# Kernel tuning notes

Measured on AMD Instinct MI355X. Metric: run time of the kernel, lower is better.

Reference implementation:

```python
import jax, jax.numpy as jnp
import numpy as np

N, E, B = 30000, 60000, 500          # nodes, edges, graphs
NODE_IN, EDGE_IN, H, R = 64, 16, 64, 1024
MP_STEPS, S2S_STEPS = 3, 3           # num_step_message_passing, num_step_set2set
D = 2 * H                            # Set2Set in_channels / LSTM hidden size


def setup_inputs() -> dict:
    key = jax.random.key(0)
    ks = jax.random.split(key, 20)
    g = lambda i, shape, s: jax.random.normal(ks[i], shape, jnp.float32) * s
    return {
        "x": g(0, (N, NODE_IN), 1.0),
        "edge_index": jax.random.randint(ks[1], (2, E), 0, N),
        "edge_attr": g(2, (E, EDGE_IN), 1.0),
        "batch": jnp.sort(jax.random.randint(ks[3], (N,), 0, B)),
        # project_node_feats
        "W_proj": g(4, (NODE_IN, H), 0.1), "b_proj": jnp.zeros((H,), jnp.float32),
        # NNConv edge network + root + bias
        "W_edge": g(5, (EDGE_IN, H * H), 0.05), "b_edge": jnp.zeros((H * H,), jnp.float32),
        "root": g(6, (H, H), 0.1), "conv_bias": jnp.zeros((H,), jnp.float32),
        # GRU (torch gate order r, z, n)
        "gru_W_ih": g(7, (3 * H, H), 0.1), "gru_W_hh": g(8, (3 * H, H), 0.1),
        "gru_b_ih": jnp.zeros((3 * H,), jnp.float32), "gru_b_hh": jnp.zeros((3 * H,), jnp.float32),
        # node classifier head
        "W_cls": g(9, (H, 1), 0.1), "b_cls": jnp.zeros((1,), jnp.float32),
        # Set2Set LSTM: input 2D (=4H), hidden D (=2H), gate order i, f, g, o
        "lstm_W_ih": g(10, (4 * D, 2 * D), 0.1), "lstm_W_hh": g(11, (4 * D, D), 0.1),
        "lstm_b_ih": jnp.zeros((4 * D,), jnp.float32), "lstm_b_hh": jnp.zeros((4 * D,), jnp.float32),
        # sparsify (Linear 4H->R + PReLU)
        "W_sp": g(12, (4 * H, R), 0.05), "b_sp": jnp.zeros((R,), jnp.float32),
        "prelu_a": jnp.float32(0.25),
        "W_y1": g(13, (R, 128), 0.05), "b_y1": jnp.zeros((128,), jnp.float32),
        "W_y2": g(14, (128, 1), 0.1), "b_y2": jnp.zeros((1,), jnp.float32),
    }


def reference(x, edge_index, edge_attr, batch,
              W_proj, b_proj, W_edge, b_edge, root, conv_bias,
              gru_W_ih, gru_W_hh, gru_b_ih, gru_b_hh,
              W_cls, b_cls,
              lstm_W_ih, lstm_W_hh, lstm_b_ih, lstm_b_hh,
              W_sp, b_sp, prelu_a, W_y1, b_y1, W_y2, b_y2):
    src, dst = edge_index[0], edge_index[1]
    h0 = jax.nn.relu(x @ W_proj + b_proj)                  # [N, H]
    # Per-edge HxH weight matrices (loop-invariant; NNConv recomputes same values).
    We = (edge_attr @ W_edge + b_edge).reshape(E, H, H)    # [E, H, H]

    node, hidden = h0, h0
    for _ in range(MP_STEPS):
        msg = jnp.einsum('eh,eho->eo', node[src], We)      # gather + per-edge matvec
        aggr = jax.ops.segment_sum(msg, dst, num_segments=N)
        m = jax.nn.relu(aggr + node @ root + conv_bias)    # NNConv output + activation
        # GRU cell (seq_len=1)
        gi = m @ gru_W_ih.T + gru_b_ih
        gh = hidden @ gru_W_hh.T + gru_b_hh
        r = jax.nn.sigmoid(gi[:, :H] + gh[:, :H])
        z = jax.nn.sigmoid(gi[:, H:2 * H] + gh[:, H:2 * H])
        n = jnp.tanh(gi[:, 2 * H:] + r * gh[:, 2 * H:])
        hidden = (1.0 - z) * n + z * hidden
        node = hidden

    xcat = jnp.concatenate([h0, node], axis=1)             # [N, 2H] = [N, D]
    p_borylation = (node @ W_cls + b_cls)[:, 0]            # [N]

    # Set2Set over xcat
    q_star = jnp.zeros((B, 2 * D), xcat.dtype)
    hs = jnp.zeros((B, D), xcat.dtype)
    cs = jnp.zeros((B, D), xcat.dtype)
    for _ in range(S2S_STEPS):
        gts = q_star @ lstm_W_ih.T + lstm_b_ih + hs @ lstm_W_hh.T + lstm_b_hh
        i_g = jax.nn.sigmoid(gts[:, :D])
        f_g = jax.nn.sigmoid(gts[:, D:2 * D])
        g_g = jnp.tanh(gts[:, 2 * D:3 * D])
        o_g = jax.nn.sigmoid(gts[:, 3 * D:])
        cs = f_g * cs + i_g * g_g
        hs = o_g * jnp.tanh(cs)
        q = hs                                             # [B, D]
        e = jnp.sum(xcat * q[batch], axis=-1)              # [N]
        mseg = jax.ops.segment_max(e, batch, num_segments=B)
        ex = jnp.exp(e - mseg[batch])
        denom = jax.ops.segment_sum(ex, batch, num_segments=B)
        a = ex / denom[batch]                              # segment softmax
        rvec = jax.ops.segment_sum(a[:, None] * xcat, batch, num_segments=B)
        q_star = jnp.concatenate([q, rvec], axis=1)        # [B, 2D] = [B, 4H]

    gf = q_star @ W_sp + b_sp
    gf = jnp.where(gf >= 0, gf, prelu_a * gf)              # PReLU
    predicted_yield = (jax.nn.relu(gf @ W_y1 + b_y1) @ W_y2 + b_y2)[:, 0]
    return p_borylation, predicted_yield
```

## Files before the change

kernel.cpp:

```cpp
#include <hip/hip_runtime.h>
#include <math.h>

#define NN 30000
#define NNP 30080
#define NE 60000
#define NB 500
#define YROW 1344

typedef __attribute__((ext_vector_type(8))) short bf16x8;
typedef __attribute__((ext_vector_type(4))) float f32x4;

__device__ __forceinline__ float sigmoidf_(float x) { return 1.0f / (1.0f + expf(-x)); }

__device__ __forceinline__ unsigned short bf_hi(float x) {
  unsigned int u = __float_as_uint(x);
  u += 0x7FFF + ((u >> 16) & 1);
  return (unsigned short)(u >> 16);
}
__device__ __forceinline__ float bf_f(unsigned short h) {
  return __uint_as_float(((unsigned int)h) << 16);
}
__device__ __forceinline__ void split_bf(float x, unsigned short& hi, unsigned short& lo) {
  hi = bf_hi(x);
  lo = bf_hi(x - bf_f(hi));
}

__device__ __forceinline__ int lower_bound_i(const int* __restrict__ a, int n, int v) {
  int lo = 0, hi = n;
  while (lo < hi) { int mid = (lo + hi) >> 1; if (a[mid] < v) lo = mid + 1; else hi = mid; }
  return lo;
}

__global__ __launch_bounds__(256) void gemm_mfma_k(
    const unsigned short* __restrict__ Ahi, const unsigned short* __restrict__ Alo,
    const unsigned short* __restrict__ Bhi, const unsigned short* __restrict__ Blo,
    float* __restrict__ C, int ldc,
    float* __restrict__ C2,
    unsigned short* __restrict__ Chi, unsigned short* __restrict__ Clo,
    const float* __restrict__ bias, int M, int flags)
{
  const int tid = threadIdx.x;
  const int wid = tid >> 6, lane = tid & 63;
  const int l15 = lane & 15, l4 = lane >> 4;
  const int r0 = blockIdx.x * 128 + (wid >> 1) * 64;
  const int c0 = blockIdx.y * 64 + (wid & 1) * 32;

  f32x4 acc[4][2];
#pragma unroll
  for (int rt = 0; rt < 4; rt++)
#pragma unroll
    for (int ct = 0; ct < 2; ct++) acc[rt][ct] = (f32x4){0.f, 0.f, 0.f, 0.f};

#pragma unroll
  for (int ks = 0; ks < 2; ks++) {
    const int kb = ks * 32 + l4 * 8;
    bf16x8 a_h[4], a_l[4], b_h[2], b_l[2];
#pragma unroll
    for (int rt = 0; rt < 4; rt++) {
      size_t off = (size_t)(r0 + rt * 16 + l15) * 64 + kb;
      a_h[rt] = *(const bf16x8*)(Ahi + off);
      a_l[rt] = *(const bf16x8*)(Alo + off);
    }
#pragma unroll
    for (int ct = 0; ct < 2; ct++) {
      size_t off = (size_t)(c0 + ct * 16 + l15) * 64 + kb;
      b_h[ct] = *(const bf16x8*)(Bhi + off);
      b_l[ct] = *(const bf16x8*)(Blo + off);
    }
#pragma unroll
    for (int rt = 0; rt < 4; rt++)
#pragma unroll
      for (int ct = 0; ct < 2; ct++) {
        acc[rt][ct] = __builtin_amdgcn_mfma_f32_16x16x32_bf16(a_h[rt], b_h[ct], acc[rt][ct], 0, 0, 0);
        acc[rt][ct] = __builtin_amdgcn_mfma_f32_16x16x32_bf16(a_h[rt], b_l[ct], acc[rt][ct], 0, 0, 0);
        acc[rt][ct] = __builtin_amdgcn_mfma_f32_16x16x32_bf16(a_l[rt], b_h[ct], acc[rt][ct], 0, 0, 0);
      }
  }

#pragma unroll
  for (int rt = 0; rt < 4; rt++) {
    const int rbase = r0 + rt * 16 + l4 * 4;
#pragma unroll
    for (int ct = 0; ct < 2; ct++) {
      const int col = c0 + ct * 16 + l15;
      const float bv = (flags & 1) ? bias[col] : 0.f;
#pragma unroll
      for (int reg = 0; reg < 4; reg++) {
        const int row = rbase + reg;
        if (row < M) {
          float v = acc[rt][ct][reg];
          if (flags & 1) v = fmaxf(v + bv, 0.f);
          C[(size_t)row * ldc + col] = v;
          if (flags & 4) C2[(size_t)row * 64 + col] = v;
          if (flags & 2) {
            unsigned short h, l;
            split_bf(v, h, l);
            Chi[(size_t)row * 64 + col] = h;
            Clo[(size_t)row * 64 + col] = l;
          }
        }
      }
    }
  }
}

__global__ __launch_bounds__(256) void prep_bt_k(
    const float* __restrict__ W_edge, const float* __restrict__ b_edge,
    const float* __restrict__ root, const float* __restrict__ gWhh,
    const float* __restrict__ gWih, const float* __restrict__ W_proj,
    unsigned short* __restrict__ BTbig_hi, unsigned short* __restrict__ BTbig_lo,
    unsigned short* __restrict__ BTih_hi, unsigned short* __restrict__ BTih_lo,
    unsigned short* __restrict__ BTp_hi, unsigned short* __restrict__ BTp_lo)
{
  int idx = blockIdx.x * 256 + threadIdx.x;
  const int NBIG = YROW * 64, NIH = 192 * 64, NP = 64 * 64;
  if (idx < NBIG) {
    int col = idx >> 6, k = idx & 63;
    float v;
    if (col < 1024) { int c = col >> 6, o2 = col & 63; v = W_edge[(size_t)c * 4096 + k * 64 + o2]; }
    else if (col < 1088) v = b_edge[k * 64 + (col - 1024)];
    else if (col < 1152) v = root[k * 64 + (col - 1088)];
    else v = gWhh[(size_t)(col - 1152) * 64 + k];
    unsigned short h, l; split_bf(v, h, l);
    BTbig_hi[idx] = h; BTbig_lo[idx] = l;
  } else if (idx < NBIG + NIH) {
    int i2 = idx - NBIG;
    float v = gWih[i2];
    unsigned short h, l; split_bf(v, h, l);
    BTih_hi[i2] = h; BTih_lo[i2] = l;
  } else if (idx < NBIG + NIH + NP) {
    int i2 = idx - NBIG - NIH;
    int o2 = i2 >> 6, k = i2 & 63;
    float v = W_proj[k * 64 + o2];
    unsigned short h, l; split_bf(v, h, l);
    BTp_hi[i2] = h; BTp_lo[i2] = l;
  }
}

__global__ __launch_bounds__(256) void prep_lstmT_k(
    const float* __restrict__ Wih, const float* __restrict__ Whh,
    float* __restrict__ Tih, float* __restrict__ Thh)
{
  int idx = blockIdx.x * 256 + threadIdx.x;
  if (idx < 256 * 512) {
    int j = idx / 512, r = idx % 512;
    Tih[idx] = Wih[(size_t)r * 256 + j];
  } else if (idx < 256 * 512 + 128 * 512) {
    int id2 = idx - 256 * 512;
    int j = id2 / 512, r = id2 % 512;
    Thh[id2] = Whh[(size_t)r * 128 + j];
  }
}

__global__ __launch_bounds__(256) void split2_k(
    const float* __restrict__ src, unsigned short* __restrict__ hi,
    unsigned short* __restrict__ lo, int n4)
{
  int i = blockIdx.x * 256 + threadIdx.x;
  if (i >= n4) return;
  float4 v = ((const float4*)src)[i];
  unsigned short h0, l0, h1, l1, h2, l2, h3, l3;
  split_bf(v.x, h0, l0); split_bf(v.y, h1, l1);
  split_bf(v.z, h2, l2); split_bf(v.w, h3, l3);
  ((ushort4*)hi)[i] = make_ushort4(h0, h1, h2, h3);
  ((ushort4*)lo)[i] = make_ushort4(l0, l1, l2, l3);
}

__global__ __launch_bounds__(256) void edge_msg_k(
    const int* __restrict__ ei, const float* __restrict__ ea, float* __restrict__ Yb)
{
  int gw = (blockIdx.x * blockDim.x + threadIdx.x) >> 6;
  if (gw >= NE) return;
  int lane = threadIdx.x & 63;
  int src = ei[gw];
  int dst = ei[NE + gw];
  const float* y = Yb + (size_t)src * YROW;
  const float* eav = ea + (size_t)gw * 16;
  float4 e0 = *(const float4*)(eav + 0);
  float4 e1 = *(const float4*)(eav + 4);
  float4 e2 = *(const float4*)(eav + 8);
  float4 e3 = *(const float4*)(eav + 12);
  float msg = y[1024 + lane];
  msg = fmaf(e0.x, y[0 * 64 + lane], msg);  msg = fmaf(e0.y, y[1 * 64 + lane], msg);
  msg = fmaf(e0.z, y[2 * 64 + lane], msg);  msg = fmaf(e0.w, y[3 * 64 + lane], msg);
  msg = fmaf(e1.x, y[4 * 64 + lane], msg);  msg = fmaf(e1.y, y[5 * 64 + lane], msg);
  msg = fmaf(e1.z, y[6 * 64 + lane], msg);  msg = fmaf(e1.w, y[7 * 64 + lane], msg);
  msg = fmaf(e2.x, y[8 * 64 + lane], msg);  msg = fmaf(e2.y, y[9 * 64 + lane], msg);
  msg = fmaf(e2.z, y[10 * 64 + lane], msg); msg = fmaf(e2.w, y[11 * 64 + lane], msg);
  msg = fmaf(e3.x, y[12 * 64 + lane], msg); msg = fmaf(e3.y, y[13 * 64 + lane], msg);
  msg = fmaf(e3.z, y[14 * 64 + lane], msg); msg = fmaf(e3.w, y[15 * 64 + lane], msg);
  atomicAdd(&Yb[(size_t)dst * YROW + 1088 + lane], msg);
}

__global__ __launch_bounds__(256) void m_relu_split_k(
    const float* __restrict__ Yb, const float* __restrict__ conv_b,
    unsigned short* __restrict__ mbh, unsigned short* __restrict__ mbl)
{
  int t = blockIdx.x * 256 + threadIdx.x;
  if (t >= NN * 64) return;
  int n = t >> 6, c = t & 63;
  float v = fmaxf(Yb[(size_t)n * YROW + 1088 + c] + conv_b[c], 0.f);
  unsigned short h, l; split_bf(v, h, l);
  mbh[t] = h; mbl[t] = l;
}

__global__ __launch_bounds__(256) void gru_split_k(
    const float* __restrict__ gi, const float* __restrict__ Yb,
    const float* __restrict__ bih, const float* __restrict__ bhh,
    float* __restrict__ h, unsigned short* __restrict__ hh, unsigned short* __restrict__ hl)
{
  int t = blockIdx.x * 256 + threadIdx.x;
  if (t >= NN * 64) return;
  int n = t >> 6, c = t & 63;
  const float* gin = gi + (size_t)n * 192;
  const float* ghn = Yb + (size_t)n * YROW + 1152;
  float r = sigmoidf_(gin[c] + bih[c] + ghn[c] + bhh[c]);
  float z = sigmoidf_(gin[64 + c] + bih[64 + c] + ghn[64 + c] + bhh[64 + c]);
  float ng = tanhf(gin[128 + c] + bih[128 + c] + r * (ghn[128 + c] + bhh[128 + c]));
  float hv = h[t];
  float hn = (1.f - z) * ng + z * hv;
  h[t] = hn;
  unsigned short hb, lb; split_bf(hn, hb, lb);
  hh[t] = hb; hl[t] = lb;
}

__global__ __launch_bounds__(256) void cls_xcat_k(
    const float* __restrict__ h, const float* __restrict__ Wcls,
    const float* __restrict__ bcls, float* __restrict__ xcat, float* __restrict__ out)
{
  int gw = (blockIdx.x * blockDim.x + threadIdx.x) >> 6;
  if (gw >= NN) return;
  int lane = threadIdx.x & 63;
  float hv = h[(size_t)gw * 64 + lane];
  xcat[(size_t)gw * 128 + 64 + lane] = hv;
  float p = hv * Wcls[lane];
#pragma unroll
  for (int off = 32; off > 0; off >>= 1) p += __shfl_xor(p, off);
  if (lane == 0) out[gw] = p + bcls[0];
}

__global__ __launch_bounds__(256) void gemmK_k(
    const float* __restrict__ A, int lda,
    const float* __restrict__ B, int ldb,
    float* __restrict__ C, int ldc,
    const float* __restrict__ Csrc,
    const float* __restrict__ bias, const float* __restrict__ alpha_p,
    int M, int K, int flags)
{
  __shared__ float As[64 * 68];
  __shared__ float Bs[64 * 64];
  const int tid = threadIdx.x;
  const int m0 = blockIdx.x * 64;
  const int n0 = blockIdx.y * 64;
  const int tx = tid & 15, ty = tid >> 4;
  float acc[4][4] = {};

  for (int kc = 0; kc < K; kc += 64) {
#pragma unroll
    for (int i = 0; i < 4; i++) {
      int f4 = tid + i * 256;
      int row = f4 >> 4;
      int kk = (f4 & 15) << 2;
      float4 v = make_float4(0.f, 0.f, 0.f, 0.f);
      if (m0 + row < M) v = *(const float4*)(A + (size_t)(m0 + row) * lda + kc + kk);
      *(float4*)&As[row * 68 + kk] = v;
    }
#pragma unroll
    for (int i = 0; i < 4; i++) {
      int f4 = tid + i * 256;
      int kk = f4 >> 4;
      int nn = (f4 & 15) << 2;
      float4 v = *(const float4*)(B + (size_t)(kc + kk) * ldb + n0 + nn);
      *(float4*)&Bs[kk * 64 + nn] = v;
    }
    __syncthreads();
    const float* As0 = As + (ty * 4 + 0) * 68;
    const float* As1 = As + (ty * 4 + 1) * 68;
    const float* As2 = As + (ty * 4 + 2) * 68;
    const float* As3 = As + (ty * 4 + 3) * 68;
#pragma unroll
    for (int k = 0; k < 64; k++) {
      float4 b = *(const float4*)(Bs + k * 64 + tx * 4);
      float a0 = As0[k], a1 = As1[k], a2 = As2[k], a3 = As3[k];
      acc[0][0] = fmaf(a0, b.x, acc[0][0]); acc[0][1] = fmaf(a0, b.y, acc[0][1]);
      acc[0][2] = fmaf(a0, b.z, acc[0][2]); acc[0][3] = fmaf(a0, b.w, acc[0][3]);
      acc[1][0] = fmaf(a1, b.x, acc[1][0]); acc[1][1] = fmaf(a1, b.y, acc[1][1]);
      acc[1][2] = fmaf(a1, b.z, acc[1][2]); acc[1][3] = fmaf(a1, b.w, acc[1][3]);
      acc[2][0] = fmaf(a2, b.x, acc[2][0]); acc[2][1] = fmaf(a2, b.y, acc[2][1]);
      acc[2][2] = fmaf(a2, b.z, acc[2][2]); acc[2][3] = fmaf(a2, b.w, acc[2][3]);
      acc[3][0] = fmaf(a3, b.x, acc[3][0]); acc[3][1] = fmaf(a3, b.y, acc[3][1]);
      acc[3][2] = fmaf(a3, b.z, acc[3][2]); acc[3][3] = fmaf(a3, b.w, acc[3][3]);
    }
    __syncthreads();
  }

  const int coln = tx * 4;
  const int col = n0 + coln;
  float alpha = (flags & 32) ? alpha_p[0] : 0.f;
#pragma unroll
  for (int i = 0; i < 4; i++) {
    int row = m0 + ty * 4 + i;
    if (row < M) {
      float v0 = acc[i][0], v1 = acc[i][1], v2 = acc[i][2], v3 = acc[i][3];
      size_t off = (size_t)row * ldc + col;
      if (flags & 4) {
        float4 s = *(const float4*)(Csrc + off);
        v0 += s.x; v1 += s.y; v2 += s.z; v3 += s.w;
      }
      if (flags & 1) {
        v0 += bias[col + 0]; v1 += bias[col + 1]; v2 += bias[col + 2]; v3 += bias[col + 3];
      }
      if (flags & 2) {
        v0 = fmaxf(v0, 0.f); v1 = fmaxf(v1, 0.f); v2 = fmaxf(v2, 0.f); v3 = fmaxf(v3, 0.f);
      }
      if (flags & 32) {
        v0 = (v0 >= 0.f) ? v0 : alpha * v0; v1 = (v1 >= 0.f) ? v1 : alpha * v1;
        v2 = (v2 >= 0.f) ? v2 : alpha * v2; v3 = (v3 >= 0.f) ? v3 : alpha * v3;
      }
      *(float4*)&C[off] = make_float4(v0, v1, v2, v3);
    }
  }
}

__global__ __launch_bounds__(256) void lstm_elem_k(
    const float* __restrict__ gts, const float* __restrict__ bih, const float* __restrict__ bhh,
    float* __restrict__ hs, float* __restrict__ cs)
{
  int t = blockIdx.x * 256 + threadIdx.x;
  if (t >= NB * 128) return;
  int b = t >> 7, d = t & 127;
  const float* g = gts + (size_t)b * 512;
  float iv = sigmoidf_(g[d] + bih[d] + bhh[d]);
  float fv = sigmoidf_(g[128 + d] + bih[128 + d] + bhh[128 + d]);
  float gv = tanhf(g[256 + d] + bih[256 + d] + bhh[256 + d]);
  float ov = sigmoidf_(g[384 + d] + bih[384 + d] + bhh[384 + d]);
  float c = fv * cs[t] + iv * gv;
  cs[t] = c;
  hs[t] = ov * tanhf(c);
}

__global__ __launch_bounds__(256) void attn_k(
    const float* __restrict__ xcat, const int* __restrict__ batch,
    const float* __restrict__ hs, float* __restrict__ e_ws, float* __restrict__ q_star)
{
  __shared__ float q[128];
  __shared__ float red[4];
  __shared__ float rvw[4 * 128];
  __shared__ float dw[4];
  __shared__ int se[2];
  int b = blockIdx.x;
  int tid = threadIdx.x;
  if (tid < 128) q[tid] = hs[(size_t)b * 128 + tid];
  if (tid == 254) se[0] = lower_bound_i(batch, NN, b);
  if (tid == 255) se[1] = lower_bound_i(batch, NN, b + 1);
  __syncthreads();
  int start = se[0], end = se[1];
  int lane = tid & 63, w = tid >> 6;
  float wmax = -INFINITY;
  for (int n = start + w; n < end; n += 4) {
    const float* xr = xcat + (size_t)n * 128;
    float p = xr[lane] * q[lane] + xr[64 + lane] * q[64 + lane];
#pragma unroll
    for (int off = 32; off > 0; off >>= 1) p += __shfl_xor(p, off);
    if (lane == 0) e_ws[n] = p;
    wmax = fmaxf(wmax, p);
  }
  if (lane == 0) red[w] = wmax;
  __syncthreads();
  float bmax = fmaxf(fmaxf(red[0], red[1]), fmaxf(red[2], red[3]));
  float a0 = 0.f, a1 = 0.f, ds = 0.f;
  for (int n = start + w; n < end; n += 4) {
    float ex = expf(e_ws[n] - bmax);
    const float* xr = xcat + (size_t)n * 128;
    a0 = fmaf(ex, xr[lane], a0);
    a1 = fmaf(ex, xr[64 + lane], a1);
    ds += ex;
  }
  rvw[w * 128 + lane] = a0;
  rvw[w * 128 + 64 + lane] = a1;
  if (lane == 0) dw[w] = ds;
  __syncthreads();
  if (tid < 128) {
    float r = rvw[tid] + rvw[128 + tid] + rvw[256 + tid] + rvw[384 + tid];
    float dsum = dw[0] + dw[1] + dw[2] + dw[3];
    q_star[(size_t)b * 256 + tid] = q[tid];
    q_star[(size_t)b * 256 + 128 + tid] = (end > start) ? (r / dsum) : 0.f;
  }
}

__global__ __launch_bounds__(256) void yout_k(
    const float* __restrict__ y1, const float* __restrict__ Wy2,
    const float* __restrict__ by2, float* __restrict__ out)
{
  int gw = (blockIdx.x * blockDim.x + threadIdx.x) >> 6;
  if (gw >= NB) return;
  int lane = threadIdx.x & 63;
  const float* yr = y1 + (size_t)gw * 128;
  float p = yr[lane] * Wy2[lane] + yr[64 + lane] * Wy2[64 + lane];
#pragma unroll
  for (int off = 32; off > 0; off >>= 1) p += __shfl_xor(p, off);
  if (lane == 0) out[gw] = p + by2[0];
}

extern "C" void kernel_launch(void* const* d_in, const int* in_sizes, int n_in,
                              void* d_out, int out_size, void* d_ws, size_t ws_size,
                              hipStream_t stream) {
  const float* x      = (const float*)d_in[0];
  const int*   ei     = (const int*)d_in[1];
  const float* ea     = (const float*)d_in[2];
  const int*   batch  = (const int*)d_in[3];
  const float* W_proj = (const float*)d_in[4];
  const float* b_proj = (const float*)d_in[5];
  const float* W_edge = (const float*)d_in[6];
  const float* b_edge = (const float*)d_in[7];
  const float* root   = (const float*)d_in[8];
  const float* conv_b = (const float*)d_in[9];
  const float* gWih   = (const float*)d_in[10];
  const float* gWhh   = (const float*)d_in[11];
  const float* gbih   = (const float*)d_in[12];
  const float* gbhh   = (const float*)d_in[13];
  const float* Wcls   = (const float*)d_in[14];
  const float* bcls   = (const float*)d_in[15];
  const float* lWih   = (const float*)d_in[16];
  const float* lWhh   = (const float*)d_in[17];
  const float* lbih   = (const float*)d_in[18];
  const float* lbhh   = (const float*)d_in[19];
  const float* Wsp    = (const float*)d_in[20];
  const float* bsp    = (const float*)d_in[21];
  const float* pa     = (const float*)d_in[22];
  const float* Wy1    = (const float*)d_in[23];
  const float* by1    = (const float*)d_in[24];
  const float* Wy2    = (const float*)d_in[25];
  const float* by2    = (const float*)d_in[26];
  float* out = (float*)d_out;

  float* ws = (float*)d_ws;
  size_t o = 0;
  float* h      = ws + o; o += (size_t)NN * 64;
  float* Ybig   = ws + o; o += (size_t)NN * YROW;
  float* gi     = ws + o; o += (size_t)NN * 192;
  float* xcat   = ws + o; o += (size_t)NN * 128;
  float* e_ws   = ws + o; o += (size_t)NN;
  float* q_star = ws + o; o += (size_t)NB * 256;
  float* hs     = ws + o; o += (size_t)NB * 128;
  float* cs     = ws + o; o += (size_t)NB * 128;
  float* Tih    = ws + o; o += 256 * 512;
  float* Thh    = ws + o; o += 128 * 512;
  float* gts    = ws + o; o += (size_t)NB * 512;
  float* gf     = ws + o; o += (size_t)NB * 1024;
  float* y1     = ws + o; o += (size_t)NB * 128;

  unsigned short* us = (unsigned short*)(ws + o);
  size_t u = 0;
  unsigned short* hh_b   = us + u; u += (size_t)NNP * 64;
  unsigned short* hl_b   = us + u; u += (size_t)NNP * 64;
  unsigned short* mbh    = us + u; u += (size_t)NNP * 64;
  unsigned short* mbl    = us + u; u += (size_t)NNP * 64;
  unsigned short* BTb_hi = us + u; u += (size_t)YROW * 64;
  unsigned short* BTb_lo = us + u; u += (size_t)YROW * 64;
  unsigned short* BTi_hi = us + u; u += (size_t)192 * 64;
  unsigned short* BTi_lo = us + u; u += (size_t)192 * 64;
  unsigned short* BTp_hi = us + u; u += (size_t)64 * 64;
  unsigned short* BTp_lo = us + u; u += (size_t)64 * 64;

  const int MT = NNP / 128;

  prep_bt_k<<<((YROW + 192 + 64) * 64 + 255) / 256, 256, 0, stream>>>(
      W_edge, b_edge, root, gWhh, gWih, W_proj,
      BTb_hi, BTb_lo, BTi_hi, BTi_lo, BTp_hi, BTp_lo);
  prep_lstmT_k<<<768, 256, 0, stream>>>(lWih, lWhh, Tih, Thh);
  split2_k<<<(NN * 16 + 255) / 256, 256, 0, stream>>>(x, hh_b, hl_b, NN * 16);

  gemm_mfma_k<<<dim3(MT, 1), 256, 0, stream>>>(hh_b, hl_b, BTp_hi, BTp_lo,
                                               xcat, 128, h, hh_b, hl_b, b_proj, NN, 1 | 2 | 4);
  for (int step = 0; step < 3; step++) {
    gemm_mfma_k<<<dim3(MT, YROW / 64), 256, 0, stream>>>(hh_b, hl_b, BTb_hi, BTb_lo,
                                                         Ybig, YROW, nullptr, nullptr, nullptr,
                                                         nullptr, NN, 0);
    edge_msg_k<<<(NE * 64) / 256, 256, 0, stream>>>(ei, ea, Ybig);
    m_relu_split_k<<<(NN * 64) / 256, 256, 0, stream>>>(Ybig, conv_b, mbh, mbl);
    gemm_mfma_k<<<dim3(MT, 3), 256, 0, stream>>>(mbh, mbl, BTi_hi, BTi_lo,
                                                 gi, 192, nullptr, nullptr, nullptr,
                                                 nullptr, NN, 0);
    gru_split_k<<<(NN * 64) / 256, 256, 0, stream>>>(gi, Ybig, gbih, gbhh, h, hh_b, hl_b);
  }
  cls_xcat_k<<<(NN * 64) / 256, 256, 0, stream>>>(h, Wcls, bcls, xcat, out);
  hipMemsetAsync(q_star, 0, (size_t)NB * (256 + 128 + 128) * sizeof(float), stream);
  for (int t = 0; t < 3; t++) {
    gemmK_k<<<dim3(8, 8), 256, 0, stream>>>(q_star, 256, Tih, 512, gts, 512,
                                            nullptr, nullptr, nullptr, NB, 256, 0);
    gemmK_k<<<dim3(8, 8), 256, 0, stream>>>(hs, 128, Thh, 512, gts, 512,
                                            gts, nullptr, nullptr, NB, 128, 4);
    lstm_elem_k<<<(NB * 128 + 255) / 256, 256, 0, stream>>>(gts, lbih, lbhh, hs, cs);
    attn_k<<<NB, 256, 0, stream>>>(xcat, batch, hs, e_ws, q_star);
  }
  gemmK_k<<<dim3(8, 16), 256, 0, stream>>>(q_star, 256, Wsp, 1024, gf, 1024,
                                           nullptr, bsp, pa, NB, 256, 1 | 32);
  gemmK_k<<<dim3(8, 2), 256, 0, stream>>>(gf, 1024, Wy1, 128, y1, 128,
                                          nullptr, by1, nullptr, NB, 1024, 1 | 2);
  yout_k<<<(NB * 64 + 255) / 256, 256, 0, stream>>>(y1, Wy2, by2, out + NN);
}
```

Baseline: 807.8 us.

## Compute NNConv messages per edge with MFMA instead of a per-node 1344-wide GEMM

Before, every node was multiplied by a 64x1344 weight matrix to produce per-channel projections, and each edge then gathered a 1344-float row. Now the node GEMM is cut to root plus GRU hidden (256 columns). A new edge kernel builds an outer-product operand (edge_attr times source h, K=1088) and multiplies it by the reordered edge-network weights with split-bf16 MFMA, then scatters the result with atomics. This removes the large Ybig write and read traffic. In exchange it adds about twice the MFMA FLOPs over edges and per-edge gathers of h.

```diff
diff --git a/kernel.cpp b/kernel.cpp
--- a/kernel.cpp
+++ b/kernel.cpp
@@ -5,7 +5,8 @@
 #define NNP 30080
 #define NE 60000
 #define NB 500
-#define YROW 1344
+#define YGH 256
+#define KE 1088
 
 typedef __attribute__((ext_vector_type(8))) short bf16x8;
 typedef __attribute__((ext_vector_type(4))) float f32x4;
@@ -104,32 +105,113 @@
   }
 }
 
+__global__ __launch_bounds__(256) void edge_mfma_k(
+    const int* __restrict__ ei, const float* __restrict__ ea,
+    const float* __restrict__ h,
+    const unsigned short* __restrict__ Whi, const unsigned short* __restrict__ Wlo,
+    float* __restrict__ Yb)
+{
+  const int tid = threadIdx.x;
+  const int wid = tid >> 6, lane = tid & 63;
+  const int l15 = lane & 15, l4 = lane >> 4;
+  const int e0 = (blockIdx.x * 4 + wid) * 64;
+
+  int srcA[4];
+  const float* eaA[4];
+#pragma unroll
+  for (int rt = 0; rt < 4; rt++) {
+    int e = e0 + rt * 16 + l15;
+    int ee = (e < NE) ? e : (NE - 1);
+    srcA[rt] = ei[ee];
+    eaA[rt] = ea + (size_t)ee * 16;
+  }
+
+  f32x4 acc[4][4];
+#pragma unroll
+  for (int rt = 0; rt < 4; rt++)
+#pragma unroll
+    for (int ct = 0; ct < 4; ct++) acc[rt][ct] = (f32x4){0.f, 0.f, 0.f, 0.f};
+
+  for (int ks = 0; ks < KE / 32; ks++) {
+    const int base = ks * 32 + l4 * 8;
+    const int c = base >> 6;
+    const int kb = base & 63;
+    bf16x8 ah[4], al[4];
+#pragma unroll
+    for (int rt = 0; rt < 4; rt++) {
+      float eac = (c < 16) ? eaA[rt][c] : 1.0f;
+      const float* hp = h + (size_t)srcA[rt] * 64 + kb;
+      float4 n0 = *(const float4*)hp;
+      float4 n1 = *(const float4*)(hp + 4);
+      float nv[8] = {n0.x, n0.y, n0.z, n0.w, n1.x, n1.y, n1.z, n1.w};
+#pragma unroll
+      for (int j = 0; j < 8; j++) {
+        unsigned short hb, lb;
+        split_bf(eac * nv[j], hb, lb);
+        ah[rt][j] = (short)hb;
+        al[rt][j] = (short)lb;
+      }
+    }
+#pragma unroll
+    for (int ct = 0; ct < 4; ct++) {
+      size_t wo = (size_t)(ct * 16 + l15) * KE + base;
+      bf16x8 bh = *(const bf16x8*)(Whi + wo);
+      bf16x8 bl = *(const bf16x8*)(Wlo + wo);
+#pragma unroll
+      for (int rt = 0; rt < 4; rt++) {
+        acc[rt][ct] = __builtin_amdgcn_mfma_f32_16x16x32_bf16(ah[rt], bh, acc[rt][ct], 0, 0, 0);
+        acc[rt][ct] = __builtin_amdgcn_mfma_f32_16x16x32_bf16(ah[rt], bl, acc[rt][ct], 0, 0, 0);
+        acc[rt][ct] = __builtin_amdgcn_mfma_f32_16x16x32_bf16(al[rt], bh, acc[rt][ct], 0, 0, 0);
+      }
+    }
+  }
+
+#pragma unroll
+  for (int rt = 0; rt < 4; rt++) {
+    const int er = e0 + rt * 16 + l4 * 4;
+#pragma unroll
+    for (int reg = 0; reg < 4; reg++) {
+      const int e = er + reg;
+      if (e < NE) {
+        const int dst = ei[NE + e];
+#pragma unroll
+        for (int ct = 0; ct < 4; ct++)
+          atomicAdd(&Yb[(size_t)dst * YGH + ct * 16 + l15], acc[rt][ct][reg]);
+      }
+    }
+  }
+}
+
 __global__ __launch_bounds__(256) void prep_bt_k(
     const float* __restrict__ W_edge, const float* __restrict__ b_edge,
     const float* __restrict__ root, const float* __restrict__ gWhh,
     const float* __restrict__ gWih, const float* __restrict__ W_proj,
     unsigned short* __restrict__ BTbig_hi, unsigned short* __restrict__ BTbig_lo,
+    unsigned short* __restrict__ W2_hi, unsigned short* __restrict__ W2_lo,
     unsigned short* __restrict__ BTih_hi, unsigned short* __restrict__ BTih_lo,
     unsigned short* __restrict__ BTp_hi, unsigned short* __restrict__ BTp_lo)
 {
   int idx = blockIdx.x * 256 + threadIdx.x;
-  const int NBIG = YROW * 64, NIH = 192 * 64, NP = 64 * 64;
+  const int NBIG = YGH * 64, NW2 = 64 * KE, NIH = 192 * 64, NP = 64 * 64;
   if (idx < NBIG) {
     int col = idx >> 6, k = idx & 63;
-    float v;
-    if (col < 1024) { int c = col >> 6, o2 = col & 63; v = W_edge[(size_t)c * 4096 + k * 64 + o2]; }
-    else if (col < 1088) v = b_edge[k * 64 + (col - 1024)];
-    else if (col < 1152) v = root[k * 64 + (col - 1088)];
-    else v = gWhh[(size_t)(col - 1152) * 64 + k];
+    float v = (col < 64) ? root[k * 64 + col] : gWhh[(size_t)(col - 64) * 64 + k];
     unsigned short h, l; split_bf(v, h, l);
     BTbig_hi[idx] = h; BTbig_lo[idx] = l;
-  } else if (idx < NBIG + NIH) {
+  } else if (idx < NBIG + NW2) {
     int i2 = idx - NBIG;
+    int o2 = i2 / KE, kq = i2 % KE;
+    int c = kq >> 6, kk = kq & 63;
+    float v = (c < 16) ? W_edge[(size_t)c * 4096 + kk * 64 + o2] : b_edge[kk * 64 + o2];
+    unsigned short h, l; split_bf(v, h, l);
+    W2_hi[i2] = h; W2_lo[i2] = l;
+  } else if (idx < NBIG + NW2 + NIH) {
+    int i2 = idx - NBIG - NW2;
     float v = gWih[i2];
     unsigned short h, l; split_bf(v, h, l);
     BTih_hi[i2] = h; BTih_lo[i2] = l;
-  } else if (idx < NBIG + NIH + NP) {
-    int i2 = idx - NBIG - NIH;
+  } else if (idx < NBIG + NW2 + NIH + NP) {
+    int i2 = idx - NBIG - NW2 - NIH;
     int o2 = i2 >> 6, k = i2 & 63;
     float v = W_proj[k * 64 + o2];
     unsigned short h, l; split_bf(v, h, l);
@@ -166,32 +248,6 @@
   ((ushort4*)lo)[i] = make_ushort4(l0, l1, l2, l3);
 }
 
-__global__ __launch_bounds__(256) void edge_msg_k(
-    const int* __restrict__ ei, const float* __restrict__ ea, float* __restrict__ Yb)
-{
-  int gw = (blockIdx.x * blockDim.x + threadIdx.x) >> 6;
-  if (gw >= NE) return;
-  int lane = threadIdx.x & 63;
-  int src = ei[gw];
-  int dst = ei[NE + gw];
-  const float* y = Yb + (size_t)src * YROW;
-  const float* eav = ea + (size_t)gw * 16;
-  float4 e0 = *(const float4*)(eav + 0);
-  float4 e1 = *(const float4*)(eav + 4);
-  float4 e2 = *(const float4*)(eav + 8);
-  float4 e3 = *(const float4*)(eav + 12);
-  float msg = y[1024 + lane];
-  msg = fmaf(e0.x, y[0 * 64 + lane], msg);  msg = fmaf(e0.y, y[1 * 64 + lane], msg);
-  msg = fmaf(e0.z, y[2 * 64 + lane], msg);  msg = fmaf(e0.w, y[3 * 64 + lane], msg);
-  msg = fmaf(e1.x, y[4 * 64 + lane], msg);  msg = fmaf(e1.y, y[5 * 64 + lane], msg);
-  msg = fmaf(e1.z, y[6 * 64 + lane], msg);  msg = fmaf(e1.w, y[7 * 64 + lane], msg);
-  msg = fmaf(e2.x, y[8 * 64 + lane], msg);  msg = fmaf(e2.y, y[9 * 64 + lane], msg);
-  msg = fmaf(e2.z, y[10 * 64 + lane], msg); msg = fmaf(e2.w, y[11 * 64 + lane], msg);
-  msg = fmaf(e3.x, y[12 * 64 + lane], msg); msg = fmaf(e3.y, y[13 * 64 + lane], msg);
-  msg = fmaf(e3.z, y[14 * 64 + lane], msg); msg = fmaf(e3.w, y[15 * 64 + lane], msg);
-  atomicAdd(&Yb[(size_t)dst * YROW + 1088 + lane], msg);
-}
-
 __global__ __launch_bounds__(256) void m_relu_split_k(
     const float* __restrict__ Yb, const float* __restrict__ conv_b,
     unsigned short* __restrict__ mbh, unsigned short* __restrict__ mbl)
@@ -199,7 +255,7 @@
   int t = blockIdx.x * 256 + threadIdx.x;
   if (t >= NN * 64) return;
   int n = t >> 6, c = t & 63;
-  float v = fmaxf(Yb[(size_t)n * YROW + 1088 + c] + conv_b[c], 0.f);
+  float v = fmaxf(Yb[(size_t)n * YGH + c] + conv_b[c], 0.f);
   unsigned short h, l; split_bf(v, h, l);
   mbh[t] = h; mbl[t] = l;
 }
@@ -213,7 +269,7 @@
   if (t >= NN * 64) return;
   int n = t >> 6, c = t & 63;
   const float* gin = gi + (size_t)n * 192;
-  const float* ghn = Yb + (size_t)n * YROW + 1152;
+  const float* ghn = Yb + (size_t)n * YGH + 64;
   float r = sigmoidf_(gin[c] + bih[c] + ghn[c] + bhh[c]);
   float z = sigmoidf_(gin[64 + c] + bih[64 + c] + ghn[64 + c] + bhh[64 + c]);
   float ng = tanhf(gin[128 + c] + bih[128 + c] + r * (ghn[128 + c] + bhh[128 + c]));
@@ -437,7 +493,7 @@
   float* ws = (float*)d_ws;
   size_t o = 0;
   float* h      = ws + o; o += (size_t)NN * 64;
-  float* Ybig   = ws + o; o += (size_t)NN * YROW;
+  float* Ybig   = ws + o; o += (size_t)NN * YGH;
   float* gi     = ws + o; o += (size_t)NN * 192;
   float* xcat   = ws + o; o += (size_t)NN * 128;
   float* e_ws   = ws + o; o += (size_t)NN;
@@ -456,28 +512,32 @@
   unsigned short* hl_b   = us + u; u += (size_t)NNP * 64;
   unsigned short* mbh    = us + u; u += (size_t)NNP * 64;
   unsigned short* mbl    = us + u; u += (size_t)NNP * 64;
-  unsigned short* BTb_hi = us + u; u += (size_t)YROW * 64;
-  unsigned short* BTb_lo = us + u; u += (size_t)YROW * 64;
+  unsigned short* BTb_hi = us + u; u += (size_t)YGH * 64;
+  unsigned short* BTb_lo = us + u; u += (size_t)YGH * 64;
+  unsigned short* W2_hi  = us + u; u += (size_t)64 * KE;
+  unsigned short* W2_lo  = us + u; u += (size_t)64 * KE;
   unsigned short* BTi_hi = us + u; u += (size_t)192 * 64;
   unsigned short* BTi_lo = us + u; u += (size_t)192 * 64;
   unsigned short* BTp_hi = us + u; u += (size_t)64 * 64;
   unsigned short* BTp_lo = us + u; u += (size_t)64 * 64;
 
   const int MT = NNP / 128;
-
-  prep_bt_k<<<((YROW + 192 + 64) * 64 + 255) / 256, 256, 0, stream>>>(
+  const int ET = (NE + 255) / 256;
+  const int PREP_N = YGH * 64 + 64 * KE + 192 * 64 + 64 * 64;
+
+  prep_bt_k<<<(PREP_N + 255) / 256, 256, 0, stream>>>(
       W_edge, b_edge, root, gWhh, gWih, W_proj,
-      BTb_hi, BTb_lo, BTi_hi, BTi_lo, BTp_hi, BTp_lo);
+      BTb_hi, BTb_lo, W2_hi, W2_lo, BTi_hi, BTi_lo, BTp_hi, BTp_lo);
   prep_lstmT_k<<<768, 256, 0, stream>>>(lWih, lWhh, Tih, Thh);
   split2_k<<<(NN * 16 + 255) / 256, 256, 0, stream>>>(x, hh_b, hl_b, NN * 16);
 
   gemm_mfma_k<<<dim3(MT, 1), 256, 0, stream>>>(hh_b, hl_b, BTp_hi, BTp_lo,
                                                xcat, 128, h, hh_b, hl_b, b_proj, NN, 1 | 2 | 4);
   for (int step = 0; step < 3; step++) {
-    gemm_mfma_k<<<dim3(MT, YROW / 64), 256, 0, stream>>>(hh_b, hl_b, BTb_hi, BTb_lo,
-                                                         Ybig, YROW, nullptr, nullptr, nullptr,
-                                                         nullptr, NN, 0);
-    edge_msg_k<<<(NE * 64) / 256, 256, 0, stream>>>(ei, ea, Ybig);
+    gemm_mfma_k<<<dim3(MT, YGH / 64), 256, 0, stream>>>(hh_b, hl_b, BTb_hi, BTb_lo,
+                                                        Ybig, YGH, nullptr, nullptr, nullptr,
+                                                        nullptr, NN, 0);
+    edge_mfma_k<<<ET, 256, 0, stream>>>(ei, ea, h, W2_hi, W2_lo, Ybig);
     m_relu_split_k<<<(NN * 64) / 256, 256, 0, stream>>>(Ybig, conv_b, mbh, mbl);
     gemm_mfma_k<<<dim3(MT, 3), 256, 0, stream>>>(mbh, mbl, BTi_hi, BTi_lo,
                                                  gi, 192, nullptr, nullptr, nullptr,
```

After: 776.2 us. 1.04x faster.
